# Optimization experiments

Hardware: AMD Instinct MI355X
Metric: run time of the kernel (lower is better)

## Reference

```python
import jax, jax.numpy as jnp
import numpy as np

B, NPG = 32, 4096   # graphs, nodes per graph (equal-size ragged segments)
F_IN, C, K, J = 64, 128, 32, 40
N_LAYERS = 3
EPS = 1e-5


def _global_layer_norm(x):
    # F.layer_norm(x, x.shape): normalize over ALL elements, no affine
    m = jnp.mean(x)
    v = jnp.mean(jnp.square(x - m))
    return (x - m) * jax.lax.rsqrt(v + EPS)


def setup_inputs() -> dict:
    key = jax.random.key(0)
    ks = jax.random.split(key, 7)
    N = B * NPG
    return {
        "node_feats": jax.random.normal(ks[0], (N, F_IN), jnp.float32),
        "frag_emb": jax.random.normal(ks[1], (B, J, F_IN), jnp.float32),
        "W_in": jax.random.normal(ks[2], (C, F_IN), jnp.float32) / np.sqrt(F_IN),
        "b_in": jnp.zeros((C,), jnp.float32),
        "U": jax.random.uniform(ks[3], (C, K), jnp.float32),
        "V": jax.random.uniform(ks[4], (C, K), jnp.float32),
        "q": jax.random.uniform(ks[5], (K,), jnp.float32),
        "gate_W": jax.random.normal(ks[6], (1, 2 * C), jnp.float32) / np.sqrt(2 * C),
        "gate_b": jnp.zeros((1,), jnp.float32),
    }


def reference(node_feats, frag_emb, W_in, b_in, U, V, q, gate_W, gate_b):
    # dropout is identity in eval mode
    xs = _global_layer_norm(node_feats @ W_in.T + b_in)      # [N, C]
    ys = _global_layer_norm(frag_emb @ W_in.T + b_in)        # [B, J, C]

    x = xs.reshape(B, NPG, C)                                # ragged segments -> [B, n, C]
    y_p = jax.nn.relu(jnp.einsum('bjd,dk->bjk', ys, V))      # [B, J, K]
    y_p = jax.nn.relu(q * y_p)

    I = x_p = None
    for il in range(N_LAYERS):
        x_p = jax.nn.relu(jnp.einsum('bid,dk->bik', x, U))   # [B, n, K]
        I = jnp.einsum('bik,bjk->bij', x_p, y_p)             # [B, n, J]
        if il < N_LAYERS - 1:
            A = jax.nn.softmax(I, axis=1)                    # softmax over nodes i
            h = jax.nn.relu(jnp.einsum('bij,bjk->bik', A, y_p))
            h = jnp.einsum('bik,dk->bid', h, V)              # [B, n, C]
            z = jax.nn.sigmoid(jnp.concatenate([x, h], -1) @ gate_W.T + gate_b)[..., 0]
            x = (1.0 - z)[..., None] * x + z[..., None] * h

    p = jnp.einsum('bij,bjk->bik', I, y_p)                   # [B, n, K]
    return jax.nn.sigmoid(jnp.einsum('bik,bik->bi', x_p, p)) # [B, n]
```

## Files before the change

kernel.cpp:

```cpp
#include <hip/hip_runtime.h>
#include <math.h>

namespace {
constexpr int BB = 32, NPG = 4096, NTOT = BB*NPG, C = 128, FIN = 64, KK = 32, JJ = 40;
constexpr int YROWS = BB*JJ;
constexpr float EPS = 1e-5f;

constexpr int CW_WU  = 0;
constexpr int CW_WV  = 2048;
constexpr int CW_VU  = 4096;
constexpr int CW_WG  = 5120;
constexpr int CW_VGX = 5184;
constexpr int CW_VGH = 5216;
constexpr int CW_CBU = 5248;
constexpr int CW_CSU = 5280;
constexpr int CW_CBV = 5312;
constexpr int CW_CSV = 5344;
constexpr int CW_SC  = 5376;
constexpr int CW_G   = 5384;
constexpr int CW_WB  = 9480;
constexpr int CW_SW  = 9544;
constexpr int CW_SB  = 9608;
constexpr int CW_SIZE = 9610;

constexpr size_t XU_OFF  = 0;
constexpr size_t GX_OFF  = XU_OFF + (size_t)NTOT*KK;
constexpr size_t YP_OFF  = GX_OFF + (size_t)NTOT;
constexpr size_t PMA_OFF = YP_OFF + (size_t)YROWS*KK;
constexpr size_t PSA_OFF = PMA_OFF + 81920;
constexpr size_t PMB_OFF = PSA_OFF + 81920;
constexpr size_t PSB_OFF = PMB_OFF + 81920;
constexpr size_t CWS_OFF = PSB_OFF + 81920;
constexpr size_t PBN_OFF = CWS_OFF + 9612;
constexpr size_t PBF_OFF = PBN_OFF + 2048;
constexpr size_t ST_OFF  = PBF_OFF + 80;
}

#define ACC8(A, wv, u0, u1) do { \
  A[0] += (wv)*(u0).x; A[1] += (wv)*(u0).y; A[2] += (wv)*(u0).z; A[3] += (wv)*(u0).w; \
  A[4] += (wv)*(u1).x; A[5] += (wv)*(u1).y; A[6] += (wv)*(u1).z; A[7] += (wv)*(u1).w; } while(0)

__global__ __launch_bounds__(256)
void k_pre(const float* __restrict__ W, const float* __restrict__ b,
           const float* __restrict__ U, const float* __restrict__ V,
           const float* __restrict__ gw, float* __restrict__ CWo) {
  __shared__ float W_l[128*64];
  __shared__ float V_l[128*32];
  const int t = threadIdx.x;
  for (int f = t; f < 2048; f += 256) *(float4*)(W_l + 4*f) = *(const float4*)(W + 4*f);
  if (blockIdx.x == 0)
    for (int f = t; f < 1024; f += 256) *(float4*)(V_l + 4*f) = *(const float4*)(V + 4*f);
  __syncthreads();
  if (blockIdx.x == 1) {
    const int d = t >> 2, e0 = (t & 3) * 16;
    float g[16];
    #pragma unroll
    for (int i = 0; i < 16; ++i) g[i] = 0.f;
    for (int c = 0; c < 128; ++c) {
      const float wv = W_l[c*64 + d];
      #pragma unroll
      for (int u = 0; u < 4; ++u) {
        const float4 we = *(const float4*)(W_l + c*64 + e0 + 4*u);
        g[4*u+0] += wv*we.x; g[4*u+1] += wv*we.y;
        g[4*u+2] += wv*we.z; g[4*u+3] += wv*we.w;
      }
    }
    #pragma unroll
    for (int u = 0; u < 4; ++u)
      *(float4*)(CWo + CW_G + d*64 + e0 + 4*u) = make_float4(g[4*u],g[4*u+1],g[4*u+2],g[4*u+3]);
    if (t < 64) {
      float awb = 0.f, asw = 0.f;
      for (int c = 0; c < 128; ++c) {
        const float wv = W_l[c*64 + t];
        awb += wv * b[c]; asw += wv;
      }
      CWo[CW_WB + t] = awb; CWo[CW_SW + t] = asw;
    }
    if (t == 0) {
      float sb = 0.f, sb2 = 0.f;
      for (int c = 0; c < 128; ++c) { sb += b[c]; sb2 += b[c]*b[c]; }
      CWo[CW_SB+0] = sb; CWo[CW_SB+1] = sb2;
    }
    return;
  }
  {
    const int d = t >> 2, k0 = (t & 3) * 8;
    float au[8] = {0,0,0,0,0,0,0,0};
    float av[8] = {0,0,0,0,0,0,0,0};
    for (int c = 0; c < 128; ++c) {
      const float wv = W_l[c*64 + d];
      const float4 u0 = *(const float4*)(U + c*32 + k0);
      const float4 u1 = *(const float4*)(U + c*32 + k0 + 4);
      ACC8(au, wv, u0, u1);
      const float4 v0 = *(const float4*)(V_l + c*32 + k0);
      const float4 v1 = *(const float4*)(V_l + c*32 + k0 + 4);
      ACC8(av, wv, v0, v1);
    }
    *(float4*)(CWo + CW_WU + d*32 + k0)     = make_float4(au[0],au[1],au[2],au[3]);
    *(float4*)(CWo + CW_WU + d*32 + k0 + 4) = make_float4(au[4],au[5],au[6],au[7]);
    *(float4*)(CWo + CW_WV + d*32 + k0)     = make_float4(av[0],av[1],av[2],av[3]);
    *(float4*)(CWo + CW_WV + d*32 + k0 + 4) = make_float4(av[4],av[5],av[6],av[7]);
  }
  if (t < 128) {
    const int kp = t >> 2, k0 = (t & 3) * 8;
    float a[8] = {0,0,0,0,0,0,0,0};
    for (int c = 0; c < 128; ++c) {
      const float vv = V_l[c*32 + kp];
      const float4 u0 = *(const float4*)(U + c*32 + k0);
      const float4 u1 = *(const float4*)(U + c*32 + k0 + 4);
      ACC8(a, vv, u0, u1);
    }
    *(float4*)(CWo + CW_VU + kp*32 + k0)     = make_float4(a[0],a[1],a[2],a[3]);
    *(float4*)(CWo + CW_VU + kp*32 + k0 + 4) = make_float4(a[4],a[5],a[6],a[7]);
  }
  if (t < 64) {
    float a = 0.f;
    for (int c = 0; c < 128; ++c) a += W_l[c*64 + t] * gw[c];
    CWo[CW_WG + t] = a;
  }
  if (t < 32) {
    float a1=0,a2=0,a3=0,a4=0,a5=0,a6=0;
    for (int c = 0; c < 128; ++c) {
      const float uv = U[c*32 + t], vv = V_l[c*32 + t], bc = b[c];
      a1 += vv*gw[c]; a2 += vv*gw[128+c];
      a3 += bc*uv;    a4 += uv;
      a5 += bc*vv;    a6 += vv;
    }
    CWo[CW_VGX+t]=a1; CWo[CW_VGH+t]=a2; CWo[CW_CBU+t]=a3; CWo[CW_CSU+t]=a4;
    CWo[CW_CBV+t]=a5; CWo[CW_CSV+t]=a6;
  }
  if (t == 0) {
    float bg=0.f, sg=0.f;
    for (int c = 0; c < 128; ++c) { bg += b[c]*gw[c]; sg += gw[c]; }
    CWo[CW_SC+0]=bg; CWo[CW_SC+1]=sg;
  }
}

__global__ __launch_bounds__(256,6)
void k_cov(const float* __restrict__ inp, const float* __restrict__ CW,
           double* __restrict__ PB, const int ntiles) {
  __shared__ float a_l[64*64];
  __shared__ float red[12];
  const int t = threadIdx.x;
  const int dg = t >> 4, eg = t & 15;
  const int d0 = dg*4, e0 = eg*4;
  float av1 = 0.f, av2 = 0.f, avb = 0.f;
  int nt = 0;
  for (int tile = blockIdx.x; tile < ntiles; tile += gridDim.x) {
    __syncthreads();
    const size_t r0 = (size_t)tile * 64;
    #pragma unroll
    for (int s = 0; s < 4; ++s) {
      int f = (t + 256*s) * 4;
      *(float4*)(a_l + f) = *(const float4*)(inp + r0*FIN + f);
    }
    __syncthreads();
    float S[4][4];
    #pragma unroll
    for (int i=0;i<4;i++)
      #pragma unroll
      for (int j=0;j<4;j++) S[i][j] = 0.f;
    float4 cs = make_float4(0.f,0.f,0.f,0.f);
    #pragma unroll 4
    for (int r = 0; r < 64; ++r) {
      const float4 ad = *(const float4*)(a_l + r*64 + d0);
      const float4 ae = *(const float4*)(a_l + r*64 + e0);
      S[0][0]+=ad.x*ae.x; S[0][1]+=ad.x*ae.y; S[0][2]+=ad.x*ae.z; S[0][3]+=ad.x*ae.w;
      S[1][0]+=ad.y*ae.x; S[1][1]+=ad.y*ae.y; S[1][2]+=ad.y*ae.z; S[1][3]+=ad.y*ae.w;
      S[2][0]+=ad.z*ae.x; S[2][1]+=ad.z*ae.y; S[2][2]+=ad.z*ae.z; S[2][3]+=ad.z*ae.w;
      S[3][0]+=ad.w*ae.x; S[3][1]+=ad.w*ae.y; S[3][2]+=ad.w*ae.z; S[3][3]+=ad.w*ae.w;
      cs.x += ad.x; cs.y += ad.y; cs.z += ad.z; cs.w += ad.w;
    }
    #pragma unroll
    for (int i = 0; i < 4; ++i) {
      const float4 g4 = *(const float4*)(CW + CW_G + (d0+i)*64 + e0);
      av2 += S[i][0]*g4.x + S[i][1]*g4.y + S[i][2]*g4.z + S[i][3]*g4.w;
    }
    if (eg == 0) {
      const float4 sw4 = *(const float4*)(CW + CW_SW + d0);
      const float4 wb4 = *(const float4*)(CW + CW_WB + d0);
      av1 += cs.x*sw4.x + cs.y*sw4.y + cs.z*sw4.z + cs.w*sw4.w;
      avb += cs.x*wb4.x + cs.y*wb4.y + cs.z*wb4.z + cs.w*wb4.w;
    }
    ++nt;
  }
  #pragma unroll
  for (int off = 32; off > 0; off >>= 1) {
    av2 += __shfl_xor(av2, off);
    av1 += __shfl_xor(av1, off);
    avb += __shfl_xor(avb, off);
  }
  const int w = t >> 6;
  if ((t & 63) == 0) { red[w*3] = av1; red[w*3+1] = av2; red[w*3+2] = avb; }
  __syncthreads();
  if (t == 0) {
    const float sb = CW[CW_SB], sb2 = CW[CW_SB+1];
    const double rowsB = 64.0 * (double)nt;
    const double s1 = (double)(red[0]+red[3]+red[6]+red[9]);
    const double s2 = (double)(red[1]+red[4]+red[7]+red[10]);
    const double sB = (double)(red[2]+red[5]+red[8]+red[11]);
    PB[(size_t)blockIdx.x*2 + 0] = s1 + rowsB*(double)sb;
    PB[(size_t)blockIdx.x*2 + 1] = s2 + 2.0*sB + rowsB*(double)sb2;
  }
}

__global__ __launch_bounds__(256)
void k_comb(const double* __restrict__ PBn, const double* __restrict__ PBf,
            double* __restrict__ ST) {
  __shared__ double red[8];
  const int t = threadIdx.x;
  double a = PBn[2*t] + PBn[2*(t+256)];
  double b = PBn[2*t+1] + PBn[2*(t+256)+1];
  #pragma unroll
  for (int off = 32; off > 0; off >>= 1) {
    a += __shfl_down(a, off);
    b += __shfl_down(b, off);
  }
  if ((t & 63) == 0) { red[(t>>6)*2] = a; red[(t>>6)*2+1] = b; }
  __syncthreads();
  if (t == 0) {
    ST[0] = red[0]+red[2]+red[4]+red[6];
    ST[1] = red[1]+red[3]+red[5]+red[7];
  }
  if (t < 64) {
    double c = (t < 20) ? PBf[2*t]   : 0.0;
    double d = (t < 20) ? PBf[2*t+1] : 0.0;
    #pragma unroll
    for (int off = 32; off > 0; off >>= 1) {
      c += __shfl_down(c, off);
      d += __shfl_down(d, off);
    }
    if (t == 0) { ST[2] = c; ST[3] = d; }
  }
}

__device__ __forceinline__ void irow_compute(const float* ypj, const float xp[8],
                                             const int kq, float4 p[10]) {
  #pragma unroll
  for (int m = 0; m < 10; ++m) {
    float4 acc;
    #pragma unroll
    for (int jj = 0; jj < 4; ++jj) {
      const int j = 4*m + jj;
      const float4 y0 = *(const float4*)(ypj + j*32 + kq*8);
      const float4 y1 = *(const float4*)(ypj + j*32 + kq*8 + 4);
      const float s = xp[0]*y0.x + xp[1]*y0.y + xp[2]*y0.z + xp[3]*y0.w
                    + xp[4]*y1.x + xp[5]*y1.y + xp[6]*y1.z + xp[7]*y1.w;
      if (jj==0) acc.x = s; else if (jj==1) acc.y = s; else if (jj==2) acc.z = s; else acc.w = s;
    }
    acc.x += __shfl_xor(acc.x,1); acc.x += __shfl_xor(acc.x,2);
    acc.y += __shfl_xor(acc.y,1); acc.y += __shfl_xor(acc.y,2);
    acc.z += __shfl_xor(acc.z,1); acc.z += __shfl_xor(acc.z,2);
    acc.w += __shfl_xor(acc.w,1); acc.w += __shfl_xor(acc.w,2);
    p[m] = acc;
  }
}

__device__ __forceinline__ void partials_out(const float4 p[10], const int t, const int kq,
    float* sredm, float* sreds, float* redm,
    float* __restrict__ PmB, float* __restrict__ PsB) {
  float ev[10];
  #pragma unroll
  for (int m = 0; m < 10; ++m) {
    const float4 qv = p[m];
    ev[m] = (kq&1) ? ((kq&2)? qv.w : qv.y) : ((kq&2)? qv.z : qv.x);
  }
  const int w = t >> 6, tl = t & 63;
  float mv[10];
  #pragma unroll
  for (int m = 0; m < 10; ++m) {
    mv[m] = ev[m];
    mv[m] = fmaxf(mv[m], __shfl_xor(mv[m], 4));
    mv[m] = fmaxf(mv[m], __shfl_xor(mv[m], 8));
    mv[m] = fmaxf(mv[m], __shfl_xor(mv[m], 16));
    mv[m] = fmaxf(mv[m], __shfl_xor(mv[m], 32));
  }
  if (tl < 4) {
    #pragma unroll
    for (int m = 0; m < 10; ++m) sredm[w*40 + 4*m + kq] = mv[m];
  }
  __syncthreads();
  if (t < 40)
    redm[t] = fmaxf(fmaxf(sredm[t], sredm[40+t]), fmaxf(sredm[80+t], sredm[120+t]));
  __syncthreads();
  float es[10];
  #pragma unroll
  for (int m = 0; m < 10; ++m) {
    const float M = redm[4*m + kq];
    es[m] = __expf(ev[m]-M);
    es[m] += __shfl_xor(es[m], 4);
    es[m] += __shfl_xor(es[m], 8);
    es[m] += __shfl_xor(es[m], 16);
    es[m] += __shfl_xor(es[m], 32);
  }
  if (tl < 4) {
    #pragma unroll
    for (int m = 0; m < 10; ++m) sreds[w*40 + 4*m + kq] = es[m];
  }
  __syncthreads();
  if (t < 40) {
    PmB[(size_t)t*64] = redm[t];
    PsB[(size_t)t*64] = sreds[t]+sreds[40+t]+sreds[80+t]+sreds[120+t];
  }
}

__global__ __launch_bounds__(256,4)
void k_yp2(const float* __restrict__ fe, const float* __restrict__ CW,
           const float* __restrict__ q, const double* __restrict__ ST,
           float* __restrict__ yp) {
  __shared__ float in_t[64*64];
  __shared__ float Wl[64*32];
  const int t = threadIdx.x;
  const int r0 = blockIdx.x * 64;
  #pragma unroll
  for (int s = 0; s < 4; ++s) {
    int f = (t + 256*s) * 4;
    int r = f >> 6, d = f & 63;
    float4 v = *(const float4*)(fe + (size_t)r0*FIN + f);
    *(float4*)(in_t + r*64 + (d ^ ((r & 7) * 8))) = v;
  }
  #pragma unroll
  for (int s = 0; s < 2; ++s) {
    int f = (t + 256*s) * 4;
    *(float4*)(Wl + f) = *(const float4*)(CW + CW_WV + f);
  }
  __syncthreads();
  const double cy = (double)YROWS * (double)C;
  const double myd = ST[2]/cy, vy = ST[3]/cy - myd*myd;
  const float ry = (float)(1.0/sqrt(vy + (double)EPS));
  const float mr = (float)myd * ry;
  const int r2 = t >> 2, kq = t & 3;
  const int swz = (r2 & 7) * 8;
  float acc[8] = {0,0,0,0,0,0,0,0};
  #pragma unroll
  for (int dc = 0; dc < 16; ++dc) {
    const int d = dc*4;
    const float4 a = *(const float4*)(in_t + r2*64 + (d ^ swz));
    { const float4 w0 = *(const float4*)(Wl + (d+0)*32 + kq*8);
      const float4 w1 = *(const float4*)(Wl + (d+0)*32 + kq*8 + 4); ACC8(acc, a.x, w0, w1); }
    { const float4 w0 = *(const float4*)(Wl + (d+1)*32 + kq*8);
      const float4 w1 = *(const float4*)(Wl + (d+1)*32 + kq*8 + 4); ACC8(acc, a.y, w0, w1); }
    { const float4 w0 = *(const float4*)(Wl + (d+2)*32 + kq*8);
      const float4 w1 = *(const float4*)(Wl + (d+2)*32 + kq*8 + 4); ACC8(acc, a.z, w0, w1); }
    { const float4 w0 = *(const float4*)(Wl + (d+3)*32 + kq*8);
      const float4 w1 = *(const float4*)(Wl + (d+3)*32 + kq*8 + 4); ACC8(acc, a.w, w0, w1); }
  }
  #pragma unroll
  for (int i = 0; i < 8; ++i) {
    const int k = kq*8 + i;
    const float typ = ry*(acc[i] + CW[CW_CBV+k]) - mr*CW[CW_CSV+k];
    float v = fmaxf(typ, 0.f);
    acc[i] = fmaxf(q[k]*v, 0.f);
  }
  *(float4*)(yp + (size_t)(r0+r2)*KK + kq*8)     = make_float4(acc[0],acc[1],acc[2],acc[3]);
  *(float4*)(yp + (size_t)(r0+r2)*KK + kq*8 + 4) = make_float4(acc[4],acc[5],acc[6],acc[7]);
}

__global__ __launch_bounds__(256,4)
void k_I0(const float* __restrict__ nf, const float* __restrict__ CW,
          const double* __restrict__ ST, const float* __restrict__ yp,
          float* __restrict__ XU, float* __restrict__ GX,
          float* __restrict__ Pm, float* __restrict__ Ps) {
  __shared__ float in_t[64*64];
  __shared__ float Wl[64*32];
  __shared__ float ypj[40*32];
  __shared__ float wgl[64];
  __shared__ float sredm[160], sreds[160], redm[40];
  const int t = threadIdx.x;
  const int bid = blockIdx.x;
  const int b = bid >> 6, blk = bid & 63;
  const size_t rowbase = (size_t)b*NPG + (size_t)blk*64;
  #pragma unroll
  for (int s = 0; s < 4; ++s) {
    int f = (t + 256*s) * 4;
    int r = f >> 6, d = f & 63;
    float4 v = *(const float4*)(nf + rowbase*FIN + f);
    *(float4*)(in_t + r*64 + (d ^ ((r & 7) * 8))) = v;
  }
  #pragma unroll
  for (int s = 0; s < 2; ++s) {
    int f = (t + 256*s) * 4;
    *(float4*)(Wl + f) = *(const float4*)(CW + CW_WU + f);
  }
  for (int f4v = t; f4v < 320; f4v += 256)
    *(float4*)(ypj + f4v*4) = *(const float4*)(yp + (size_t)b*(JJ*KK) + f4v*4);
  if (t < 64) wgl[t] = CW[CW_WG + t];
  __syncthreads();
  const double cx = (double)NTOT * (double)C;
  const double mx = ST[0]/cx, vx = ST[1]/cx - mx*mx;
  const float rx = (float)(1.0/sqrt(vx + (double)EPS));
  const float mr = (float)mx * rx;
  const int r2 = t >> 2, kq = t & 3;
  const int swz = (r2 & 7) * 8;
  float acc[8] = {0,0,0,0,0,0,0,0};
  #pragma unroll
  for (int dc = 0; dc < 16; ++dc) {
    const int d = dc*4;
    const float4 a = *(const float4*)(in_t + r2*64 + (d ^ swz));
    { const float4 w0 = *(const float4*)(Wl + (d+0)*32 + kq*8);
      const float4 w1 = *(const float4*)(Wl + (d+0)*32 + kq*8 + 4); ACC8(acc, a.x, w0, w1); }
    { const float4 w0 = *(const float4*)(Wl + (d+1)*32 + kq*8);
      const float4 w1 = *(const float4*)(Wl + (d+1)*32 + kq*8 + 4); ACC8(acc, a.y, w0, w1); }
    { const float4 w0 = *(const float4*)(Wl + (d+2)*32 + kq*8);
      const float4 w1 = *(const float4*)(Wl + (d+2)*32 + kq*8 + 4); ACC8(acc, a.z, w0, w1); }
    { const float4 w0 = *(const float4*)(Wl + (d+3)*32 + kq*8);
      const float4 w1 = *(const float4*)(Wl + (d+3)*32 + kq*8 + 4); ACC8(acc, a.w, w0, w1); }
  }
  float gp = 0.f;
  #pragma unroll
  for (int u = 0; u < 4; ++u) {
    const int d = kq*16 + 4*u;
    const float4 a = *(const float4*)(in_t + r2*64 + (d ^ swz));
    const float4 w = *(const float4*)(wgl + d);
    gp += a.x*w.x + a.y*w.y + a.z*w.z + a.w*w.w;
  }
  gp += __shfl_xor(gp, 1); gp += __shfl_xor(gp, 2);
  float xp[8];
  #pragma unroll
  for (int i = 0; i < 8; ++i) {
    const int k = kq*8 + i;
    const float xv = rx*(acc[i] + CW[CW_CBU+k]) - mr*CW[CW_CSU+k];
    acc[i] = xv;
    xp[i] = fmaxf(xv, 0.f);
  }
  *(float4*)(XU + (rowbase+r2)*KK + kq*8)     = make_float4(acc[0],acc[1],acc[2],acc[3]);
  *(float4*)(XU + (rowbase+r2)*KK + kq*8 + 4) = make_float4(acc[4],acc[5],acc[6],acc[7]);
  if (kq == 0) GX[rowbase + r2] = rx*(gp + CW[CW_SC+0]) - mr*CW[CW_SC+1];
  float4 p[10];
  irow_compute(ypj, xp, kq, p);
  partials_out(p, t, kq, sredm, sreds, redm,
               Pm + (size_t)b*2560 + blk, Ps + (size_t)b*2560 + blk);
}

template<int FINAL>
__global__ __launch_bounds__(256,4)
void k_fused2(float* __restrict__ XU, float* __restrict__ GX,
              const float* __restrict__ yp, const float* __restrict__ CW,
              const float* __restrict__ gb,
              const float* __restrict__ PmIn, const float* __restrict__ PsIn,
              float* __restrict__ PmOut, float* __restrict__ PsOut,
              float* __restrict__ outp) {
  __shared__ float ypj[40*32];
  __shared__ float e_l[64*44];
  __shared__ float h_l[64*40];
  __shared__ float VUl[32*32];
  __shared__ float M_l[40], Si_l[40];
  __shared__ float vgxl[32], vghl[32];
  float* sredm = e_l;
  float* sreds = e_l + 160;
  float* redm  = e_l + 320;
  const int t = threadIdx.x;
  const int bid = blockIdx.x;
  const int b = bid >> 6, blk = bid & 63;
  const size_t rowbase = (size_t)b*NPG + (size_t)blk*64;
  for (int f4v = t; f4v < 640; f4v += 256) {
    const int j = f4v >> 4;
    const int c0 = (4*f4v) & 63;
    const float4 pm4 = *(const float4*)(PmIn + (size_t)b*2560 + 4*f4v);
    const float4 ps4 = *(const float4*)(PsIn + (size_t)b*2560 + 4*f4v);
    e_l[(c0+0)*40 + j] = pm4.x; e_l[(c0+1)*40 + j] = pm4.y;
    e_l[(c0+2)*40 + j] = pm4.z; e_l[(c0+3)*40 + j] = pm4.w;
    h_l[(c0+0)*40 + j] = ps4.x; h_l[(c0+1)*40 + j] = ps4.y;
    h_l[(c0+2)*40 + j] = ps4.z; h_l[(c0+3)*40 + j] = ps4.w;
  }
  for (int f4v = t; f4v < 320; f4v += 256)
    *(float4*)(ypj + f4v*4) = *(const float4*)(yp + (size_t)b*(JJ*KK) + f4v*4);
  *(float4*)(VUl + 4*t) = *(const float4*)(CW + CW_VU + 4*t);
  if (t < 32) { vgxl[t] = CW[CW_VGX+t]; vghl[t] = CW[CW_VGH+t]; }
  __syncthreads();
  if (t < 40) {
    float M = 0.f;
    for (int k2 = 0; k2 < 64; ++k2) M = fmaxf(M, e_l[k2*40 + t]);
    float S = 0.f;
    for (int k2 = 0; k2 < 64; ++k2) S += h_l[k2*40 + t]*__expf(e_l[k2*40 + t]-M);
    M_l[t] = M; Si_l[t] = 1.f/S;
  }
  const int r2 = t >> 2, kq = t & 3;
  float xu[8];
  {
    const float4 x0 = *(const float4*)(XU + (rowbase+r2)*KK + kq*8);
    const float4 x1 = *(const float4*)(XU + (rowbase+r2)*KK + kq*8 + 4);
    xu[0]=x0.x; xu[1]=x0.y; xu[2]=x0.z; xu[3]=x0.w;
    xu[4]=x1.x; xu[5]=x1.y; xu[6]=x1.z; xu[7]=x1.w;
  }
  const float gx = GX[rowbase + r2];
  float xp[8];
  #pragma unroll
  for (int i = 0; i < 8; ++i) xp[i] = fmaxf(xu[i], 0.f);
  __syncthreads();
  float4 p[10];
  irow_compute(ypj, xp, kq, p);
  #pragma unroll
  for (int m = 0; m < 10; ++m) {
    if ((m & 3) == kq) {
      float4 e4;
      e4.x = __expf(p[m].x - M_l[4*m+0]) * Si_l[4*m+0];
      e4.y = __expf(p[m].y - M_l[4*m+1]) * Si_l[4*m+1];
      e4.z = __expf(p[m].z - M_l[4*m+2]) * Si_l[4*m+2];
      e4.w = __expf(p[m].w - M_l[4*m+3]) * Si_l[4*m+3];
      *(float4*)(e_l + r2*44 + 4*m) = e4;
    }
  }
  __syncthreads();
  {
    const int rq = t >> 3, kc = t & 7;
    float4 h0 = make_float4(0.f,0.f,0.f,0.f), h1 = make_float4(0.f,0.f,0.f,0.f);
    #pragma unroll 4
    for (int j = 0; j < JJ; ++j) {
      const float4 yv = *(const float4*)(ypj + j*32 + kc*4);
      const float e0 = e_l[rq*44 + j];
      const float e1 = e_l[(rq+32)*44 + j];
      h0.x += e0*yv.x; h0.y += e0*yv.y; h0.z += e0*yv.z; h0.w += e0*yv.w;
      h1.x += e1*yv.x; h1.y += e1*yv.y; h1.z += e1*yv.z; h1.w += e1*yv.w;
    }
    h0.x = fmaxf(h0.x,0.f); h0.y = fmaxf(h0.y,0.f); h0.z = fmaxf(h0.z,0.f); h0.w = fmaxf(h0.w,0.f);
    h1.x = fmaxf(h1.x,0.f); h1.y = fmaxf(h1.y,0.f); h1.z = fmaxf(h1.z,0.f); h1.w = fmaxf(h1.w,0.f);
    *(float4*)(h_l + rq*40 + kc*4) = h0;
    *(float4*)(h_l + (rq+32)*40 + kc*4) = h1;
  }
  __syncthreads();
  float hu[8] = {0,0,0,0,0,0,0,0};
  float gh2 = 0.f, ghx = 0.f;
  #pragma unroll 8
  for (int kp = 0; kp < KK; ++kp) {
    const float hv = h_l[r2*40 + kp];
    gh2 += hv * vghl[kp];
    ghx += hv * vgxl[kp];
    const float4 v0 = *(const float4*)(VUl + kp*32 + kq*8);
    const float4 v1 = *(const float4*)(VUl + kp*32 + kq*8 + 4);
    ACC8(hu, hv, v0, v1);
  }
  const float z = 1.f/(1.f + __expf(-(gx + gh2 + gb[0])));
  #pragma unroll
  for (int i = 0; i < 8; ++i) {
    xu[i] = (1.f - z)*xu[i] + z*hu[i];
    xp[i] = fmaxf(xu[i], 0.f);
  }
  if (!FINAL) {
    *(float4*)(XU + (rowbase+r2)*KK + kq*8)     = make_float4(xu[0],xu[1],xu[2],xu[3]);
    *(float4*)(XU + (rowbase+r2)*KK + kq*8 + 4) = make_float4(xu[4],xu[5],xu[6],xu[7]);
    if (kq == 0) GX[rowbase + r2] = (1.f - z)*gx + z*ghx;
  }
  irow_compute(ypj, xp, kq, p);
  if (FINAL) {
    float s = 0.f;
    #pragma unroll
    for (int m = 0; m < 10; ++m)
      s += p[m].x*p[m].x + p[m].y*p[m].y + p[m].z*p[m].z + p[m].w*p[m].w;
    if (kq == 0) outp[rowbase + r2] = 1.f/(1.f + __expf(-s));
    return;
  }
  partials_out(p, t, kq, sredm, sreds, redm,
               PmOut + (size_t)b*2560 + blk, PsOut + (size_t)b*2560 + blk);
}

extern "C" void kernel_launch(void* const* d_in, const int* in_sizes, int n_in,
                              void* d_out, int out_size, void* d_ws, size_t ws_size,
                              hipStream_t stream) {
  const float* nf  = (const float*)d_in[0];
  const float* fe  = (const float*)d_in[1];
  const float* W   = (const float*)d_in[2];
  const float* bin = (const float*)d_in[3];
  const float* U   = (const float*)d_in[4];
  const float* V   = (const float*)d_in[5];
  const float* q   = (const float*)d_in[6];
  const float* gw  = (const float*)d_in[7];
  const float* gb  = (const float*)d_in[8];
  float* out = (float*)d_out;
  float* wf  = (float*)d_ws;

  float* XU  = wf + XU_OFF;
  float* GX  = wf + GX_OFF;
  float* YP  = wf + YP_OFF;
  float* PMa = wf + PMA_OFF;
  float* PSa = wf + PSA_OFF;
  float* PMb = wf + PMB_OFF;
  float* PSb = wf + PSB_OFF;
  float* CWp = wf + CWS_OFF;
  double* PBn = (double*)(wf + PBN_OFF);
  double* PBf = (double*)(wf + PBF_OFF);
  double* ST  = (double*)(wf + ST_OFF);

  k_pre<<<2, 256, 0, stream>>>(W, bin, U, V, gw, CWp);
  k_cov<<<512, 256, 0, stream>>>(nf, CWp, PBn, NTOT/64);
  k_cov<<<20, 256, 0, stream>>>(fe, CWp, PBf, YROWS/64);
  k_comb<<<1, 256, 0, stream>>>(PBn, PBf, ST);
  k_yp2<<<YROWS/64, 256, 0, stream>>>(fe, CWp, q, ST, YP);
  k_I0<<<NTOT/64, 256, 0, stream>>>(nf, CWp, ST, YP, XU, GX, PMa, PSa);
  k_fused2<0><<<NTOT/64, 256, 0, stream>>>(XU, GX, YP, CWp, gb, PMa, PSa, PMb, PSb, nullptr);
  k_fused2<1><<<NTOT/64, 256, 0, stream>>>(XU, GX, YP, CWp, gb, PMb, PSb, nullptr, nullptr, out);
}
```

Measured before the change: 290.4 us.

## Register-tile four rows per thread and hoist softmax stat combine into separate kernel

Restructures the node kernels so each thread computes four rows and splits the J and D dimensions across lanes. This improves reuse of LDS-loaded weights and yp values, and padded LDS strides replace the XOR swizzle. The per-block combination of softmax max/sum partials, previously recomputed by all 2048 blocks, moves into a small 32-block k_comb2 kernel that writes M and 1/S per graph. The h and gating computation is reorganized into register-accumulated passes with shuffle reductions. The cost is more registers per thread, two extra kernel launches, and added shuffles and syncs.

```diff
diff --git a/kernel.cpp b/kernel.cpp
--- a/kernel.cpp
+++ b/kernel.cpp
@@ -33,12 +33,22 @@
 constexpr size_t CWS_OFF = PSB_OFF + 81920;
 constexpr size_t PBN_OFF = CWS_OFF + 9612;
 constexpr size_t PBF_OFF = PBN_OFF + 2048;
-constexpr size_t ST_OFF  = PBF_OFF + 80;
+constexpr size_t MS_OFF  = PBF_OFF + 80;
+constexpr size_t ST_OFF  = MS_OFF + 2560;
 }
 
 #define ACC8(A, wv, u0, u1) do { \
   A[0] += (wv)*(u0).x; A[1] += (wv)*(u0).y; A[2] += (wv)*(u0).z; A[3] += (wv)*(u0).w; \
   A[4] += (wv)*(u1).x; A[5] += (wv)*(u1).y; A[6] += (wv)*(u1).z; A[7] += (wv)*(u1).w; } while(0)
+
+__device__ __forceinline__ float dot4(const float4 a, const float4 b) {
+  return a.x*b.x + a.y*b.y + a.z*b.z + a.w*b.w;
+}
+__device__ __forceinline__ float dot8v(const float x[8], const float4 y0, const float4 y1) {
+  return x[0]*y0.x + x[1]*y0.y + x[2]*y0.z + x[3]*y0.w
+       + x[4]*y1.x + x[5]*y1.y + x[6]*y1.z + x[7]*y1.w;
+}
+__device__ __forceinline__ float sigm(const float x) { return 1.f/(1.f + __expf(-x)); }
 
 __global__ __launch_bounds__(256)
 void k_pre(const float* __restrict__ W, const float* __restrict__ b,
@@ -234,38 +244,70 @@
   }
 }
 
-__device__ __forceinline__ void irow_compute(const float* ypj, const float xp[8],
-                                             const int kq, float4 p[10]) {
-  #pragma unroll
-  for (int m = 0; m < 10; ++m) {
-    float4 acc;
-    #pragma unroll
-    for (int jj = 0; jj < 4; ++jj) {
-      const int j = 4*m + jj;
-      const float4 y0 = *(const float4*)(ypj + j*32 + kq*8);
-      const float4 y1 = *(const float4*)(ypj + j*32 + kq*8 + 4);
-      const float s = xp[0]*y0.x + xp[1]*y0.y + xp[2]*y0.z + xp[3]*y0.w
-                    + xp[4]*y1.x + xp[5]*y1.y + xp[6]*y1.z + xp[7]*y1.w;
-      if (jj==0) acc.x = s; else if (jj==1) acc.y = s; else if (jj==2) acc.z = s; else acc.w = s;
-    }
-    acc.x += __shfl_xor(acc.x,1); acc.x += __shfl_xor(acc.x,2);
-    acc.y += __shfl_xor(acc.y,1); acc.y += __shfl_xor(acc.y,2);
-    acc.z += __shfl_xor(acc.z,1); acc.z += __shfl_xor(acc.z,2);
-    acc.w += __shfl_xor(acc.w,1); acc.w += __shfl_xor(acc.w,2);
-    p[m] = acc;
-  }
-}
-
-__device__ __forceinline__ void partials_out(const float4 p[10], const int t, const int kq,
+__global__ __launch_bounds__(256)
+void k_comb2(const float* __restrict__ Pm, const float* __restrict__ Ps,
+             float* __restrict__ MS) {
+  __shared__ float Mq[160], Sq[160], Msh[40];
+  const int t = threadIdx.x;
+  const int b = blockIdx.x;
+  const int j = t >> 2, q = t & 3;
+  float pm[16];
+  if (t < 160) {
+    float m = 0.f;
+    #pragma unroll
+    for (int u = 0; u < 16; ++u) {
+      pm[u] = Pm[(size_t)b*2560 + j*64 + q*16 + u];
+      m = fmaxf(m, pm[u]);
+    }
+    Mq[t] = m;
+  }
+  __syncthreads();
+  if (t < 40) Msh[t] = fmaxf(fmaxf(Mq[4*t], Mq[4*t+1]), fmaxf(Mq[4*t+2], Mq[4*t+3]));
+  __syncthreads();
+  if (t < 160) {
+    const float M = Msh[j];
+    float s = 0.f;
+    #pragma unroll
+    for (int u = 0; u < 16; ++u)
+      s += Ps[(size_t)b*2560 + j*64 + q*16 + u] * __expf(pm[u] - M);
+    Sq[t] = s;
+  }
+  __syncthreads();
+  if (t < 40) {
+    const float S = Sq[4*t] + Sq[4*t+1] + Sq[4*t+2] + Sq[4*t+3];
+    MS[(size_t)b*80 + t] = Msh[t];
+    MS[(size_t)b*80 + 40 + t] = 1.f/S;
+  }
+}
+
+__device__ __forceinline__ void irow4(const float* ypj, const int kq, const int jh,
+                                      const float xp[4][8], float p[4][10]) {
+  #pragma unroll
+  for (int jj = 0; jj < 10; ++jj) {
+    const int j = jh*10 + jj;
+    const float4 y0 = *(const float4*)(ypj + j*40 + kq*8);
+    const float4 y1 = *(const float4*)(ypj + j*40 + kq*8 + 4);
+    #pragma unroll
+    for (int i = 0; i < 4; ++i)
+      p[i][jj] = dot8v(xp[i], y0, y1);
+  }
+  #pragma unroll
+  for (int i = 0; i < 4; ++i)
+    #pragma unroll
+    for (int jj = 0; jj < 10; ++jj) {
+      p[i][jj] += __shfl_xor(p[i][jj], 1);
+      p[i][jj] += __shfl_xor(p[i][jj], 2);
+    }
+}
+
+__device__ __forceinline__ void partials_lds(const float* p_l, const int t,
     float* sredm, float* sreds, float* redm,
     float* __restrict__ PmB, float* __restrict__ PsB) {
+  const int r2 = t >> 2, kq = t & 3;
+  const int w = t >> 6, tl = t & 63;
   float ev[10];
   #pragma unroll
-  for (int m = 0; m < 10; ++m) {
-    const float4 qv = p[m];
-    ev[m] = (kq&1) ? ((kq&2)? qv.w : qv.y) : ((kq&2)? qv.z : qv.x);
-  }
-  const int w = t >> 6, tl = t & 63;
+  for (int m = 0; m < 10; ++m) ev[m] = p_l[r2*44 + 4*m + kq];
   float mv[10];
   #pragma unroll
   for (int m = 0; m < 10; ++m) {
@@ -357,15 +399,16 @@
 }
 
 __global__ __launch_bounds__(256,4)
-void k_I0(const float* __restrict__ nf, const float* __restrict__ CW,
-          const double* __restrict__ ST, const float* __restrict__ yp,
-          float* __restrict__ XU, float* __restrict__ GX,
-          float* __restrict__ Pm, float* __restrict__ Ps) {
-  __shared__ float in_t[64*64];
-  __shared__ float Wl[64*32];
-  __shared__ float ypj[40*32];
-  __shared__ float wgl[64];
+void k_I0b(const float* __restrict__ nf, const float* __restrict__ CW,
+           const double* __restrict__ ST, const float* __restrict__ yp,
+           float* __restrict__ XU, float* __restrict__ GX,
+           float* __restrict__ Pm, float* __restrict__ Ps) {
+  __shared__ __align__(16) float in_t[64*68];
+  __shared__ __align__(16) float Wl[64*36];
+  __shared__ __align__(16) float ypj[40*40];
+  __shared__ __align__(16) float wgl[64];
   __shared__ float sredm[160], sreds[160], redm[40];
+  float* p_l = in_t;
   const int t = threadIdx.x;
   const int bid = blockIdx.x;
   const int b = bid >> 6, blk = bid & 63;
@@ -374,183 +417,265 @@
   for (int s = 0; s < 4; ++s) {
     int f = (t + 256*s) * 4;
     int r = f >> 6, d = f & 63;
-    float4 v = *(const float4*)(nf + rowbase*FIN + f);
-    *(float4*)(in_t + r*64 + (d ^ ((r & 7) * 8))) = v;
+    *(float4*)(in_t + r*68 + d) = *(const float4*)(nf + rowbase*FIN + f);
   }
   #pragma unroll
   for (int s = 0; s < 2; ++s) {
-    int f = (t + 256*s) * 4;
-    *(float4*)(Wl + f) = *(const float4*)(CW + CW_WU + f);
-  }
-  for (int f4v = t; f4v < 320; f4v += 256)
-    *(float4*)(ypj + f4v*4) = *(const float4*)(yp + (size_t)b*(JJ*KK) + f4v*4);
+    int idx = t + 256*s;
+    int d = idx >> 3, kc = idx & 7;
+    *(float4*)(Wl + ((d&15)*4 + (d>>4))*36 + kc*4) = *(const float4*)(CW + CW_WU + idx*4);
+  }
+  for (int f4v = t; f4v < 320; f4v += 256) {
+    int j = f4v >> 3, kc = f4v & 7;
+    *(float4*)(ypj + j*40 + kc*4) = *(const float4*)(yp + (size_t)b*(JJ*KK) + f4v*4);
+  }
   if (t < 64) wgl[t] = CW[CW_WG + t];
   __syncthreads();
   const double cx = (double)NTOT * (double)C;
   const double mx = ST[0]/cx, vx = ST[1]/cx - mx*mx;
   const float rx = (float)(1.0/sqrt(vx + (double)EPS));
   const float mr = (float)mx * rx;
-  const int r2 = t >> 2, kq = t & 3;
-  const int swz = (r2 & 7) * 8;
-  float acc[8] = {0,0,0,0,0,0,0,0};
-  #pragma unroll
-  for (int dc = 0; dc < 16; ++dc) {
-    const int d = dc*4;
-    const float4 a = *(const float4*)(in_t + r2*64 + (d ^ swz));
-    { const float4 w0 = *(const float4*)(Wl + (d+0)*32 + kq*8);
-      const float4 w1 = *(const float4*)(Wl + (d+0)*32 + kq*8 + 4); ACC8(acc, a.x, w0, w1); }
-    { const float4 w0 = *(const float4*)(Wl + (d+1)*32 + kq*8);
-      const float4 w1 = *(const float4*)(Wl + (d+1)*32 + kq*8 + 4); ACC8(acc, a.y, w0, w1); }
-    { const float4 w0 = *(const float4*)(Wl + (d+2)*32 + kq*8);
-      const float4 w1 = *(const float4*)(Wl + (d+2)*32 + kq*8 + 4); ACC8(acc, a.z, w0, w1); }
-    { const float4 w0 = *(const float4*)(Wl + (d+3)*32 + kq*8);
-      const float4 w1 = *(const float4*)(Wl + (d+3)*32 + kq*8 + 4); ACC8(acc, a.w, w0, w1); }
-  }
-  float gp = 0.f;
-  #pragma unroll
-  for (int u = 0; u < 4; ++u) {
-    const int d = kq*16 + 4*u;
-    const float4 a = *(const float4*)(in_t + r2*64 + (d ^ swz));
-    const float4 w = *(const float4*)(wgl + d);
-    gp += a.x*w.x + a.y*w.y + a.z*w.z + a.w*w.w;
-  }
-  gp += __shfl_xor(gp, 1); gp += __shfl_xor(gp, 2);
-  float xp[8];
-  #pragma unroll
-  for (int i = 0; i < 8; ++i) {
-    const int k = kq*8 + i;
-    const float xv = rx*(acc[i] + CW[CW_CBU+k]) - mr*CW[CW_CSU+k];
-    acc[i] = xv;
-    xp[i] = fmaxf(xv, 0.f);
-  }
-  *(float4*)(XU + (rowbase+r2)*KK + kq*8)     = make_float4(acc[0],acc[1],acc[2],acc[3]);
-  *(float4*)(XU + (rowbase+r2)*KK + kq*8 + 4) = make_float4(acc[4],acc[5],acc[6],acc[7]);
-  if (kq == 0) GX[rowbase + r2] = rx*(gp + CW[CW_SC+0]) - mr*CW[CW_SC+1];
-  float4 p[10];
-  irow_compute(ypj, xp, kq, p);
-  partials_out(p, t, kq, sredm, sreds, redm,
+  const int kq = t & 3, X = (t >> 2) & 3, rr = t >> 4;
+  float acc[4][8];
+  #pragma unroll
+  for (int i=0;i<4;i++)
+    #pragma unroll
+    for (int u=0;u<8;u++) acc[i][u] = 0.f;
+  #pragma unroll
+  for (int dd = 0; dd < 4; ++dd) {
+    float4 a4[4];
+    #pragma unroll
+    for (int i = 0; i < 4; ++i)
+      a4[i] = *(const float4*)(in_t + (rr+16*i)*68 + X*16 + dd*4);
+    #pragma unroll
+    for (int qd = 0; qd < 4; ++qd) {
+      const int lrow = (dd*4 + qd)*4 + X;
+      const float4 w0 = *(const float4*)(Wl + lrow*36 + kq*8);
+      const float4 w1 = *(const float4*)(Wl + lrow*36 + kq*8 + 4);
+      #pragma unroll
+      for (int i = 0; i < 4; ++i) {
+        const float av = (qd==0)? a4[i].x : (qd==1)? a4[i].y : (qd==2)? a4[i].z : a4[i].w;
+        ACC8(acc[i], av, w0, w1);
+      }
+    }
+  }
+  #pragma unroll
+  for (int i = 0; i < 4; ++i)
+    #pragma unroll
+    for (int u = 0; u < 8; ++u) {
+      acc[i][u] += __shfl_xor(acc[i][u], 4);
+      acc[i][u] += __shfl_xor(acc[i][u], 8);
+    }
+  float gp[4];
+  #pragma unroll
+  for (int i = 0; i < 4; ++i) {
+    const float4 a = *(const float4*)(in_t + (rr+16*i)*68 + X*16 + kq*4);
+    const float4 w = *(const float4*)(wgl + X*16 + kq*4);
+    gp[i] = dot4(a, w);
+    gp[i] += __shfl_xor(gp[i], 1);
+    gp[i] += __shfl_xor(gp[i], 2);
+    gp[i] += __shfl_xor(gp[i], 4);
+    gp[i] += __shfl_xor(gp[i], 8);
+  }
+  const float4 cb0 = *(const float4*)(CW + CW_CBU + kq*8);
+  const float4 cb1 = *(const float4*)(CW + CW_CBU + kq*8 + 4);
+  const float4 cu0 = *(const float4*)(CW + CW_CSU + kq*8);
+  const float4 cu1 = *(const float4*)(CW + CW_CSU + kq*8 + 4);
+  float xp[4][8];
+  #pragma unroll
+  for (int i = 0; i < 4; ++i) {
+    acc[i][0] = rx*(acc[i][0] + cb0.x) - mr*cu0.x;
+    acc[i][1] = rx*(acc[i][1] + cb0.y) - mr*cu0.y;
+    acc[i][2] = rx*(acc[i][2] + cb0.z) - mr*cu0.z;
+    acc[i][3] = rx*(acc[i][3] + cb0.w) - mr*cu0.w;
+    acc[i][4] = rx*(acc[i][4] + cb1.x) - mr*cu1.x;
+    acc[i][5] = rx*(acc[i][5] + cb1.y) - mr*cu1.y;
+    acc[i][6] = rx*(acc[i][6] + cb1.z) - mr*cu1.z;
+    acc[i][7] = rx*(acc[i][7] + cb1.w) - mr*cu1.w;
+    #pragma unroll
+    for (int u = 0; u < 8; ++u) xp[i][u] = fmaxf(acc[i][u], 0.f);
+  }
+  if (X == 0) {
+    const float bG = CW[CW_SC], sG = CW[CW_SC+1];
+    #pragma unroll
+    for (int i = 0; i < 4; ++i) {
+      const size_t row = rowbase + rr + 16*i;
+      *(float4*)(XU + row*KK + kq*8)     = make_float4(acc[i][0],acc[i][1],acc[i][2],acc[i][3]);
+      *(float4*)(XU + row*KK + kq*8 + 4) = make_float4(acc[i][4],acc[i][5],acc[i][6],acc[i][7]);
+      if (kq == 0) GX[row] = rx*(gp[i] + bG) - mr*sG;
+    }
+  }
+  float p[4][10];
+  irow4(ypj, kq, X, xp, p);
+  __syncthreads();
+  if (kq == 0) {
+    #pragma unroll
+    for (int i = 0; i < 4; ++i)
+      #pragma unroll
+      for (int u = 0; u < 5; ++u)
+        *(float2*)(p_l + (rr+16*i)*44 + X*10 + 2*u) = make_float2(p[i][2*u], p[i][2*u+1]);
+  }
+  __syncthreads();
+  partials_lds(p_l, t, sredm, sreds, redm,
                Pm + (size_t)b*2560 + blk, Ps + (size_t)b*2560 + blk);
 }
 
 template<int FINAL>
 __global__ __launch_bounds__(256,4)
-void k_fused2(float* __restrict__ XU, float* __restrict__ GX,
+void k_fused3(float* __restrict__ XU, float* __restrict__ GX,
               const float* __restrict__ yp, const float* __restrict__ CW,
-              const float* __restrict__ gb,
-              const float* __restrict__ PmIn, const float* __restrict__ PsIn,
+              const float* __restrict__ gb, const float* __restrict__ MS,
               float* __restrict__ PmOut, float* __restrict__ PsOut,
               float* __restrict__ outp) {
-  __shared__ float ypj[40*32];
-  __shared__ float e_l[64*44];
-  __shared__ float h_l[64*40];
-  __shared__ float VUl[32*32];
+  __shared__ __align__(16) float ypj[40*40];
+  __shared__ __align__(16) float xp_l[64*36];
+  __shared__ __align__(16) float BUF[3456];
+  __shared__ __align__(16) float vg_l[64];
   __shared__ float M_l[40], Si_l[40];
-  __shared__ float vgxl[32], vghl[32];
-  float* sredm = e_l;
-  float* sreds = e_l + 160;
-  float* redm  = e_l + 320;
+  __shared__ float sredm[160], sreds[160], redm[40];
+  float* h_l  = BUF;
+  float* VU_l = BUF + 2304;
+  float* p_l  = BUF;
   const int t = threadIdx.x;
   const int bid = blockIdx.x;
   const int b = bid >> 6, blk = bid & 63;
   const size_t rowbase = (size_t)b*NPG + (size_t)blk*64;
-  for (int f4v = t; f4v < 640; f4v += 256) {
-    const int j = f4v >> 4;
-    const int c0 = (4*f4v) & 63;
-    const float4 pm4 = *(const float4*)(PmIn + (size_t)b*2560 + 4*f4v);
-    const float4 ps4 = *(const float4*)(PsIn + (size_t)b*2560 + 4*f4v);
-    e_l[(c0+0)*40 + j] = pm4.x; e_l[(c0+1)*40 + j] = pm4.y;
-    e_l[(c0+2)*40 + j] = pm4.z; e_l[(c0+3)*40 + j] = pm4.w;
-    h_l[(c0+0)*40 + j] = ps4.x; h_l[(c0+1)*40 + j] = ps4.y;
-    h_l[(c0+2)*40 + j] = ps4.z; h_l[(c0+3)*40 + j] = ps4.w;
-  }
-  for (int f4v = t; f4v < 320; f4v += 256)
-    *(float4*)(ypj + f4v*4) = *(const float4*)(yp + (size_t)b*(JJ*KK) + f4v*4);
-  *(float4*)(VUl + 4*t) = *(const float4*)(CW + CW_VU + 4*t);
-  if (t < 32) { vgxl[t] = CW[CW_VGX+t]; vghl[t] = CW[CW_VGH+t]; }
-  __syncthreads();
-  if (t < 40) {
-    float M = 0.f;
-    for (int k2 = 0; k2 < 64; ++k2) M = fmaxf(M, e_l[k2*40 + t]);
-    float S = 0.f;
-    for (int k2 = 0; k2 < 64; ++k2) S += h_l[k2*40 + t]*__expf(e_l[k2*40 + t]-M);
-    M_l[t] = M; Si_l[t] = 1.f/S;
-  }
-  const int r2 = t >> 2, kq = t & 3;
-  float xu[8];
+  for (int f4v = t; f4v < 320; f4v += 256) {
+    int j = f4v >> 3, kc = f4v & 7;
+    *(float4*)(ypj + j*40 + kc*4) = *(const float4*)(yp + (size_t)b*(JJ*KK) + f4v*4);
+  }
   {
-    const float4 x0 = *(const float4*)(XU + (rowbase+r2)*KK + kq*8);
-    const float4 x1 = *(const float4*)(XU + (rowbase+r2)*KK + kq*8 + 4);
-    xu[0]=x0.x; xu[1]=x0.y; xu[2]=x0.z; xu[3]=x0.w;
-    xu[4]=x1.x; xu[5]=x1.y; xu[6]=x1.z; xu[7]=x1.w;
-  }
-  const float gx = GX[rowbase + r2];
-  float xp[8];
-  #pragma unroll
-  for (int i = 0; i < 8; ++i) xp[i] = fmaxf(xu[i], 0.f);
-  __syncthreads();
-  float4 p[10];
-  irow_compute(ypj, xp, kq, p);
-  #pragma unroll
-  for (int m = 0; m < 10; ++m) {
-    if ((m & 3) == kq) {
-      float4 e4;
-      e4.x = __expf(p[m].x - M_l[4*m+0]) * Si_l[4*m+0];
-      e4.y = __expf(p[m].y - M_l[4*m+1]) * Si_l[4*m+1];
-      e4.z = __expf(p[m].z - M_l[4*m+2]) * Si_l[4*m+2];
-      e4.w = __expf(p[m].w - M_l[4*m+3]) * Si_l[4*m+3];
-      *(float4*)(e_l + r2*44 + 4*m) = e4;
+    const int d = t >> 3, kc = t & 7;
+    *(float4*)(VU_l + d*36 + kc*4) = *(const float4*)(CW + CW_VU + t*4);
+  }
+  if (t < 32) vg_l[t] = CW[CW_VGX + t];
+  else if (t < 64) vg_l[t] = CW[CW_VGH + t - 32];
+  if (t < 40) { M_l[t] = MS[(size_t)b*80 + t]; Si_l[t] = MS[(size_t)b*80 + 40 + t]; }
+  __syncthreads();
+  const int kq = t & 3, jh = (t >> 2) & 3, rr = t >> 4;
+  float xp[4][8];
+  #pragma unroll
+  for (int i = 0; i < 4; ++i) {
+    const size_t row = rowbase + rr + 16*i;
+    const float4 x0 = *(const float4*)(XU + row*KK + kq*8);
+    const float4 x1 = *(const float4*)(XU + row*KK + kq*8 + 4);
+    xp[i][0]=fmaxf(x0.x,0.f); xp[i][1]=fmaxf(x0.y,0.f);
+    xp[i][2]=fmaxf(x0.z,0.f); xp[i][3]=fmaxf(x0.w,0.f);
+    xp[i][4]=fmaxf(x1.x,0.f); xp[i][5]=fmaxf(x1.y,0.f);
+    xp[i][6]=fmaxf(x1.z,0.f); xp[i][7]=fmaxf(x1.w,0.f);
+  }
+  float p[4][10];
+  irow4(ypj, kq, jh, xp, p);
+  float hp[4][8];
+  #pragma unroll
+  for (int i=0;i<4;i++)
+    #pragma unroll
+    for (int u=0;u<8;u++) hp[i][u] = 0.f;
+  #pragma unroll
+  for (int jj = 0; jj < 10; ++jj) {
+    const int j = jh*10 + jj;
+    const float Mj = M_l[j], Sj = Si_l[j];
+    const float4 y0 = *(const float4*)(ypj + j*40 + kq*8);
+    const float4 y1 = *(const float4*)(ypj + j*40 + kq*8 + 4);
+    #pragma unroll
+    for (int i = 0; i < 4; ++i) {
+      const float e = __expf(p[i][jj] - Mj) * Sj;
+      ACC8(hp[i], e, y0, y1);
+    }
+  }
+  #pragma unroll
+  for (int i = 0; i < 4; ++i)
+    #pragma unroll
+    for (int u = 0; u < 8; ++u) {
+      hp[i][u] += __shfl_xor(hp[i][u], 4);
+      hp[i][u] += __shfl_xor(hp[i][u], 8);
+    }
+  if (jh == 0) {
+    #pragma unroll
+    for (int i = 0; i < 4; ++i) {
+      const int rl = rr + 16*i;
+      *(float4*)(h_l + rl*36 + kq*8) =
+        make_float4(fmaxf(hp[i][0],0.f), fmaxf(hp[i][1],0.f),
+                    fmaxf(hp[i][2],0.f), fmaxf(hp[i][3],0.f));
+      *(float4*)(h_l + rl*36 + kq*8 + 4) =
+        make_float4(fmaxf(hp[i][4],0.f), fmaxf(hp[i][5],0.f),
+                    fmaxf(hp[i][6],0.f), fmaxf(hp[i][7],0.f));
     }
   }
   __syncthreads();
   {
-    const int rq = t >> 3, kc = t & 7;
-    float4 h0 = make_float4(0.f,0.f,0.f,0.f), h1 = make_float4(0.f,0.f,0.f,0.f);
-    #pragma unroll 4
-    for (int j = 0; j < JJ; ++j) {
-      const float4 yv = *(const float4*)(ypj + j*32 + kc*4);
-      const float e0 = e_l[rq*44 + j];
-      const float e1 = e_l[(rq+32)*44 + j];
-      h0.x += e0*yv.x; h0.y += e0*yv.y; h0.z += e0*yv.z; h0.w += e0*yv.w;
-      h1.x += e1*yv.x; h1.y += e1*yv.y; h1.z += e1*yv.z; h1.w += e1*yv.w;
-    }
-    h0.x = fmaxf(h0.x,0.f); h0.y = fmaxf(h0.y,0.f); h0.z = fmaxf(h0.z,0.f); h0.w = fmaxf(h0.w,0.f);
-    h1.x = fmaxf(h1.x,0.f); h1.y = fmaxf(h1.y,0.f); h1.z = fmaxf(h1.z,0.f); h1.w = fmaxf(h1.w,0.f);
-    *(float4*)(h_l + rq*40 + kc*4) = h0;
-    *(float4*)(h_l + (rq+32)*40 + kc*4) = h1;
-  }
-  __syncthreads();
-  float hu[8] = {0,0,0,0,0,0,0,0};
-  float gh2 = 0.f, ghx = 0.f;
-  #pragma unroll 8
-  for (int kp = 0; kp < KK; ++kp) {
-    const float hv = h_l[r2*40 + kp];
-    gh2 += hv * vghl[kp];
-    ghx += hv * vgxl[kp];
-    const float4 v0 = *(const float4*)(VUl + kp*32 + kq*8);
-    const float4 v1 = *(const float4*)(VUl + kp*32 + kq*8 + 4);
-    ACC8(hu, hv, v0, v1);
-  }
-  const float z = 1.f/(1.f + __expf(-(gx + gh2 + gb[0])));
-  #pragma unroll
-  for (int i = 0; i < 8; ++i) {
-    xu[i] = (1.f - z)*xu[i] + z*hu[i];
-    xp[i] = fmaxf(xu[i], 0.f);
-  }
-  if (!FINAL) {
-    *(float4*)(XU + (rowbase+r2)*KK + kq*8)     = make_float4(xu[0],xu[1],xu[2],xu[3]);
-    *(float4*)(XU + (rowbase+r2)*KK + kq*8 + 4) = make_float4(xu[4],xu[5],xu[6],xu[7]);
-    if (kq == 0) GX[rowbase + r2] = (1.f - z)*gx + z*ghx;
-  }
-  irow_compute(ypj, xp, kq, p);
+    const int kk2 = t & 15, rr2 = t >> 4;
+    float hu0[4] = {0,0,0,0}, hu1[4] = {0,0,0,0};
+    float g2[4] = {0,0,0,0}, gxp[4] = {0,0,0,0};
+    #pragma unroll
+    for (int c8 = 0; c8 < 8; ++c8) {
+      const float4 vgx4 = *(const float4*)(vg_l + c8*4);
+      const float4 vgh4 = *(const float4*)(vg_l + 32 + c8*4);
+      float2 vu[4];
+      #pragma unroll
+      for (int qd = 0; qd < 4; ++qd)
+        vu[qd] = *(const float2*)(VU_l + (c8*4+qd)*36 + kk2*2);
+      #pragma unroll
+      for (int i = 0; i < 4; ++i) {
+        const float4 h4 = *(const float4*)(h_l + (rr2+16*i)*36 + c8*4);
+        g2[i]  += dot4(h4, vgh4);
+        gxp[i] += dot4(h4, vgx4);
+        hu0[i] += h4.x*vu[0].x + h4.y*vu[1].x + h4.z*vu[2].x + h4.w*vu[3].x;
+        hu1[i] += h4.x*vu[0].y + h4.y*vu[1].y + h4.z*vu[2].y + h4.w*vu[3].y;
+      }
+    }
+    const float gbv = gb[0];
+    #pragma unroll
+    for (int i = 0; i < 4; ++i) {
+      const size_t row = rowbase + rr2 + 16*i;
+      const float gx = GX[row];
+      const float2 xu2 = *(const float2*)(XU + row*KK + kk2*2);
+      const float z = sigm(gx + g2[i] + gbv);
+      const float nx0 = (1.f-z)*xu2.x + z*hu0[i];
+      const float nx1 = (1.f-z)*xu2.y + z*hu1[i];
+      if (!FINAL) {
+        *(float2*)(XU + row*KK + kk2*2) = make_float2(nx0, nx1);
+        if (kk2 == 0) GX[row] = (1.f-z)*gx + z*gxp[i];
+      }
+      *(float2*)(xp_l + (rr2+16*i)*36 + kk2*2) = make_float2(fmaxf(nx0,0.f), fmaxf(nx1,0.f));
+    }
+  }
+  __syncthreads();
+  #pragma unroll
+  for (int i = 0; i < 4; ++i) {
+    const int rl = rr + 16*i;
+    const float4 x0 = *(const float4*)(xp_l + rl*36 + kq*8);
+    const float4 x1 = *(const float4*)(xp_l + rl*36 + kq*8 + 4);
+    xp[i][0]=x0.x; xp[i][1]=x0.y; xp[i][2]=x0.z; xp[i][3]=x0.w;
+    xp[i][4]=x1.x; xp[i][5]=x1.y; xp[i][6]=x1.z; xp[i][7]=x1.w;
+  }
+  irow4(ypj, kq, jh, xp, p);
   if (FINAL) {
-    float s = 0.f;
-    #pragma unroll
-    for (int m = 0; m < 10; ++m)
-      s += p[m].x*p[m].x + p[m].y*p[m].y + p[m].z*p[m].z + p[m].w*p[m].w;
-    if (kq == 0) outp[rowbase + r2] = 1.f/(1.f + __expf(-s));
+    float s[4];
+    #pragma unroll
+    for (int i = 0; i < 4; ++i) {
+      s[i] = 0.f;
+      #pragma unroll
+      for (int jj = 0; jj < 10; ++jj) s[i] += p[i][jj]*p[i][jj];
+      s[i] += __shfl_xor(s[i], 4);
+      s[i] += __shfl_xor(s[i], 8);
+    }
+    if ((t & 15) == 0) {
+      #pragma unroll
+      for (int i = 0; i < 4; ++i)
+        outp[rowbase + rr + 16*i] = sigm(s[i]);
+    }
     return;
   }
-  partials_out(p, t, kq, sredm, sreds, redm,
+  if (kq == 0) {
+    #pragma unroll
+    for (int i = 0; i < 4; ++i)
+      #pragma unroll
+      for (int u = 0; u < 5; ++u)
+        *(float2*)(p_l + (rr+16*i)*44 + jh*10 + 2*u) = make_float2(p[i][2*u], p[i][2*u+1]);
+  }
+  __syncthreads();
+  partials_lds(p_l, t, sredm, sreds, redm,
                PmOut + (size_t)b*2560 + blk, PsOut + (size_t)b*2560 + blk);
 }
 
@@ -577,6 +702,7 @@
   float* PMb = wf + PMB_OFF;
   float* PSb = wf + PSB_OFF;
   float* CWp = wf + CWS_OFF;
+  float* MSb = wf + MS_OFF;
   double* PBn = (double*)(wf + PBN_OFF);
   double* PBf = (double*)(wf + PBF_OFF);
   double* ST  = (double*)(wf + ST_OFF);
@@ -586,7 +712,9 @@
   k_cov<<<20, 256, 0, stream>>>(fe, CWp, PBf, YROWS/64);
   k_comb<<<1, 256, 0, stream>>>(PBn, PBf, ST);
   k_yp2<<<YROWS/64, 256, 0, stream>>>(fe, CWp, q, ST, YP);
-  k_I0<<<NTOT/64, 256, 0, stream>>>(nf, CWp, ST, YP, XU, GX, PMa, PSa);
-  k_fused2<0><<<NTOT/64, 256, 0, stream>>>(XU, GX, YP, CWp, gb, PMa, PSa, PMb, PSb, nullptr);
-  k_fused2<1><<<NTOT/64, 256, 0, stream>>>(XU, GX, YP, CWp, gb, PMb, PSb, nullptr, nullptr, out);
-}
+  k_I0b<<<NTOT/64, 256, 0, stream>>>(nf, CWp, ST, YP, XU, GX, PMa, PSa);
+  k_comb2<<<32, 256, 0, stream>>>(PMa, PSa, MSb);
+  k_fused3<0><<<NTOT/64, 256, 0, stream>>>(XU, GX, YP, CWp, gb, MSb, PMb, PSb, nullptr);
+  k_comb2<<<32, 256, 0, stream>>>(PMb, PSb, MSb);
+  k_fused3<1><<<NTOT/64, 256, 0, stream>>>(XU, GX, YP, CWp, gb, MSb, nullptr, nullptr, out);
+}
```

New measurement: 439.2 us. +51.3%, slower.
